# Kernel tuning notes

Measured on AMD Instinct MI355X. Metric: run time of the kernel, lower is better.

Reference implementation:

```python
import jax, jax.numpy as jnp
import numpy as np
from jax import lax

M, B, L, Q, S = 4, 64, 512, 512, 26  # models, batch, seq_len, hmm states, alphabet


def setup_inputs() -> dict:
    key = jax.random.key(0)
    k1, k2, k3, k4 = jax.random.split(key, 4)
    inputs = jax.random.uniform(k1, (M, B, L, S), dtype=jnp.float32)
    A_logits = jax.random.normal(k2, (M, Q, Q), dtype=jnp.float32)
    init_logits = jax.random.normal(k3, (M, Q), dtype=jnp.float32)
    em_logits = jax.random.normal(k4, (M, Q, S), dtype=jnp.float32)
    return {"inputs": inputs, "A_logits": A_logits,
            "init_logits": init_logits, "em_logits": em_logits}


def reference(inputs, A_logits, init_logits, em_logits):
    """Profile-HMM forward algorithm (scaled), as run by the MsaHmmCell RNN.

    inputs:      [M, B, L, S] observation probabilities (one-hot or soft)
    A_logits:    [M, Q, Q]    transition logits (row-softmax -> stochastic A)
    init_logits: [M, Q]       initial state distribution logits
    em_logits:   [M, Q, S]    emission logits (softmax over alphabet)
    returns loglik [M, B]  (the tensor the layer returns)
    """
    A = jax.nn.softmax(A_logits, axis=-1)        # [M, Q, Q]
    pi = jax.nn.softmax(init_logits, axis=-1)    # [M, Q]
    Bem = jax.nn.softmax(em_logits, axis=-1)     # [M, Q, S]

    # per-step emission likelihoods, time-major for scan: [L, M, B, Q]
    E = jnp.einsum('mbls,mqs->lmbq', inputs, Bem)

    # t = 0: alpha_0 = pi * e_0, scaled
    a0 = pi[:, None, :] * E[0]                   # [M, B, Q]
    s0 = jnp.sum(a0, axis=-1, keepdims=True)
    carry0 = (a0 / s0, jnp.log(s0[..., 0]))      # (alpha [M,B,Q], loglik [M,B])

    def step(carry, e_t):
        alpha, ll = carry
        r = jnp.einsum('mbq,mqp->mbp', alpha, A)  # transition
        a = r * e_t                               # emission
        s = jnp.sum(a, axis=-1, keepdims=True)    # scaling factor
        return (a / s, ll + jnp.log(s[..., 0])), None

    (alpha, loglik), _ = lax.scan(step, carry0, E[1:])
    return loglik  # [M, B] == reshape(loglik, (num_models, -1)) in the layer
```

## Files before the change

kernel.cpp:

```cpp
#include <hip/hip_runtime.h>
#include <hip/hip_bf16.h>
#include <math.h>


#define MM 4
#define BB 64
#define LL 512
#define QQ 512
#define SS 26
#define ASTR 528

typedef float f32x4 __attribute__((ext_vector_type(4)));
typedef int i32x4 __attribute__((ext_vector_type(4)));
typedef int i32x8 __attribute__((ext_vector_type(8)));

__device__ __forceinline__ float bf2f(unsigned short u) {
    return __uint_as_float(((unsigned)u) << 16);
}
__device__ __forceinline__ unsigned short f2bf(float f) {
    unsigned u = __float_as_uint(f);
    u = u + 0x7FFFu + ((u >> 16) & 1u);
    return (unsigned short)(u >> 16);
}
__device__ __forceinline__ unsigned char f2fp8(float x) {
    int r = __builtin_amdgcn_cvt_pk_fp8_f32(x, x, 0, false);
    return (unsigned char)(r & 0xFF);
}
__device__ __forceinline__ i32x8 ld32B(const unsigned char* p) {
    i32x4 lo = *(const i32x4*)p;
    i32x4 hi = *(const i32x4*)(p + 16);
    return __builtin_shufflevector(lo, hi, 0, 1, 2, 3, 4, 5, 6, 7);
}
__device__ __forceinline__ void barrier_lds() {
    __asm__ __volatile__("" ::: "memory");
    __builtin_amdgcn_s_waitcnt(0xC07F);
    __builtin_amdgcn_s_barrier();
    __asm__ __volatile__("" ::: "memory");
}


__global__ void prep_small(const float* __restrict__ il, const float* __restrict__ em,
                           float* __restrict__ pi, float* __restrict__ Bem) {
    int blk = blockIdx.x;
    int m = blk / (QQ + 1);
    int r = blk % (QQ + 1);
    int lane = threadIdx.x;
    if (r < QQ) {
        float x = (lane < SS) ? em[((size_t)m * QQ + r) * SS + lane] : -1e30f;
        float mx = x;
        #pragma unroll
        for (int o = 1; o < 64; o <<= 1) mx = fmaxf(mx, __shfl_xor(mx, o));
        float e = (lane < SS) ? __expf(x - mx) : 0.f;
        float s = e;
        #pragma unroll
        for (int o = 1; o < 64; o <<= 1) s += __shfl_xor(s, o);
        if (lane < SS) Bem[((size_t)m * QQ + r) * SS + lane] = e / s;
    } else {
        float v[8];
        float mx = -1e30f;
        #pragma unroll
        for (int k = 0; k < 8; ++k) { v[k] = il[m * QQ + k * 64 + lane]; mx = fmaxf(mx, v[k]); }
        #pragma unroll
        for (int o = 1; o < 64; o <<= 1) mx = fmaxf(mx, __shfl_xor(mx, o));
        float s = 0.f;
        #pragma unroll
        for (int k = 0; k < 8; ++k) { v[k] = __expf(v[k] - mx); s += v[k]; }
        #pragma unroll
        for (int o = 1; o < 64; o <<= 1) s += __shfl_xor(s, o);
        #pragma unroll
        for (int k = 0; k < 8; ++k) pi[m * QQ + k * 64 + lane] = v[k] / s;
    }
}

__global__ void prep_arow(const float* __restrict__ Al, float* __restrict__ Lrow) {
    int row = blockIdx.x;
    int lane = threadIdx.x;
    const float* p = Al + (size_t)row * QQ;
    float v[8];
    float mx = -1e30f;
    #pragma unroll
    for (int k = 0; k < 8; ++k) { v[k] = p[k * 64 + lane]; mx = fmaxf(mx, v[k]); }
    #pragma unroll
    for (int o = 1; o < 64; o <<= 1) mx = fmaxf(mx, __shfl_xor(mx, o));
    float s = 0.f;
    #pragma unroll
    for (int k = 0; k < 8; ++k) s += __expf(v[k] - mx);
    #pragma unroll
    for (int o = 1; o < 64; o <<= 1) s += __shfl_xor(s, o);
    if (lane == 0) Lrow[row] = mx + __logf(s);
}

__global__ void prep_atq(const float* __restrict__ Al, const float* __restrict__ Lrow,
                         unsigned char* __restrict__ Atq) {
    int bid = blockIdx.x;
    int m = bid >> 3, pb = bid & 7;
    __shared__ unsigned char tile[64][68];
    int l6 = threadIdx.x & 63, g = threadIdx.x >> 6;
    for (int c = 0; c < 8; ++c) {
        #pragma unroll
        for (int r = 0; r < 16; ++r) {
            int ql = g * 16 + r;
            int q = c * 64 + ql;
            float x = Al[((size_t)m * QQ + q) * QQ + pb * 64 + l6];
            tile[ql][l6] = f2fp8(__expf(x - Lrow[m * QQ + q]) * 256.f);
        }
        __syncthreads();
        #pragma unroll
        for (int r = 0; r < 16; ++r) {
            int pr = g * 16 + r;
            Atq[((size_t)m * QQ + pb * 64 + pr) * QQ + c * 64 + l6] = tile[l6][pr];
        }
        __syncthreads();
    }
}

__global__ void prep_e(const float* __restrict__ inp, const float* __restrict__ Bem,
                       unsigned short* __restrict__ E) {
    int bid = blockIdx.x;
    int tc = bid & 7;
    int b = (bid >> 3) & 63;
    int m = bid >> 9;
    int q0 = threadIdx.x;
    float bem0[SS], bem1[SS];
    const float* bp = Bem + (size_t)m * QQ * SS;
    #pragma unroll
    for (int j = 0; j < SS; ++j) bem0[j] = bp[(size_t)q0 * SS + j];
    #pragma unroll
    for (int j = 0; j < SS; ++j) bem1[j] = bp[(size_t)(q0 + 256) * SS + j];
    const float* ip = inp + (((size_t)(m * BB + b)) * LL + tc * 64) * SS;
    for (int lt = 0; lt < 64; ++lt) {
        int t = tc * 64 + lt;
        float a0 = 0.f, a1 = 0.f;
        #pragma unroll
        for (int j = 0; j < SS; ++j) {
            float x = ip[lt * SS + j];
            a0 += x * bem0[j];
            a1 += x * bem1[j];
        }
        size_t o = (((size_t)m * LL + t) * BB + b) * QQ + q0;
        E[o] = f2bf(a0);
        E[o + 256] = f2bf(a1);
    }
}


__launch_bounds__(1024, 4)
__global__ void hmm_scan(const unsigned short* __restrict__ E,
                         const unsigned char* __restrict__ Atq,
                         const float* __restrict__ pi,
                         float* __restrict__ out) {
    const int c = blockIdx.x;
    const int m = c >> 2, bg = c & 3;
    const int tid = threadIdx.x;
    const int lane = tid & 63;
    const int wv = tid >> 6;
    const int sl = lane & 15;
    const int quad = lane >> 4;
    const float LOG256 = 5.545177444479562f;

    __shared__ unsigned char albuf[2][16 * ASTR];
    __shared__ float psl[2][16][36];
    __shared__ float Sfin[2][16];

    i32x8 breg[2][4];
    {
        const unsigned char* Ab = Atq + (size_t)m * QQ * QQ;
        #pragma unroll
        for (int h = 0; h < 2; ++h) {
            int p = wv * 32 + h * 16 + sl;
            const unsigned char* rp = Ab + (size_t)p * QQ + quad * 32;
            #pragma unroll
            for (int kc = 0; kc < 4; ++kc)
                breg[h][kc] = ld32B(rp + kc * 128);
        }
    }

    int wq[2];
    #pragma unroll
    for (int h = 0; h < 2; ++h)
        wq[h] = sl * ASTR + wv * 32 + h * 16 + quad * 4;

    const int b = bg * 16 + sl;
    const size_t ebase = (size_t)m * LL * BB * QQ;
    const ushort4* __restrict__ E4 = (const ushort4*)(E + ebase);
    const unsigned ESTR4 = (BB * QQ) >> 2;
    const unsigned ebq = (unsigned)(b * QQ) >> 2;
    const unsigned eoffs0 = (unsigned)(wv * 8 + quad);
    const unsigned eoffs1 = eoffs0 + 4;

    float v[2][4];
    ushort4 ea[2], eb[2];

    {
        ea[0] = E4[ebq + ESTR4 + eoffs0];
        ea[1] = E4[ebq + ESTR4 + eoffs1];
        #pragma unroll
        for (int h = 0; h < 2; ++h) {
            int p0 = wv * 32 + h * 16 + quad * 4;
            f32x4 pv = *(const f32x4*)(pi + m * QQ + p0);
            ushort4 e0 = E4[ebq + (h ? eoffs1 : eoffs0)];
            v[h][0] = pv[0] * bf2f(e0.x);
            v[h][1] = pv[1] * bf2f(e0.y);
            v[h][2] = pv[2] * bf2f(e0.z);
            v[h][3] = pv[3] * bf2f(e0.w);
        }
    }

    float lam = 0.5f;
    float gprev = 1.0f;
    float ll = 0.0f;

    auto body = [&](int t, ushort4 (&ecur)[2], ushort4 (&enxt)[2], unsigned epre) {
        const int par = t & 1;
        enxt[0] = E4[epre + eoffs0];
        enxt[1] = E4[epre + eoffs1];

        float g = 128.0f * __builtin_amdgcn_rcpf(lam);
        unsigned char* ab = &albuf[par][0];
        #pragma unroll
        for (int h = 0; h < 2; ++h) {
            int d = __builtin_amdgcn_cvt_pk_fp8_f32(g * v[h][0], g * v[h][1], 0, false);
            d = __builtin_amdgcn_cvt_pk_fp8_f32(g * v[h][2], g * v[h][3], d, true);
            *(int*)(ab + wq[h]) = d;
        }
        float ps = (v[0][0] + v[0][1]) + (v[0][2] + v[0][3])
                 + (v[1][0] + v[1][1]) + (v[1][2] + v[1][3]);
        ps += __shfl_xor(ps, 16);
        if ((quad & 1) == 0) psl[par][sl][2 * wv + (quad >> 1)] = ps;

        ll -= __logf(g) + LOG256;

        barrier_lds();

        if (wv == 0 && lane < 32) {
            const f32x4* pr = (const f32x4*)&psl[par][sl][(lane >> 4) * 16];
            f32x4 s0 = pr[0], s1 = pr[1], s2 = pr[2], s3 = pr[3];
            f32x4 ss4 = (s0 + s1) + (s2 + s3);
            float ss = (ss4[0] + ss4[1]) + (ss4[2] + ss4[3]);
            ss += __shfl_xor(ss, 16);
            if (lane < 16) Sfin[par][sl] = ss;
        }
        if (t == 0) {
            lam = 16384.0f;
        } else {
            float Sp = Sfin[par ^ 1][sl];
            lam = 16384.0f * g * gprev * Sp;
        }
        gprev = g;

        f32x4 acc[2];
        acc[0] = (f32x4){0.f, 0.f, 0.f, 0.f};
        acc[1] = (f32x4){0.f, 0.f, 0.f, 0.f};
        const unsigned char* ar = &albuf[par][0] + sl * ASTR + quad * 32;
        #pragma unroll
        for (int kc = 0; kc < 4; ++kc) {
            i32x8 af = ld32B(ar + kc * 128);
            #pragma unroll
            for (int h = 0; h < 2; ++h)
                acc[h] = __builtin_amdgcn_mfma_scale_f32_16x16x128_f8f6f4(
                    breg[h][kc], af, acc[h], 0, 0,
                    0, 0x7F7F7F7F, 0, 0x7F7F7F7F);
        }
        #pragma unroll
        for (int h = 0; h < 2; ++h) {
            v[h][0] = acc[h][0] * bf2f(ecur[h].x);
            v[h][1] = acc[h][1] * bf2f(ecur[h].y);
            v[h][2] = acc[h][2] * bf2f(ecur[h].z);
            v[h][3] = acc[h][3] * bf2f(ecur[h].w);
        }
    };

    unsigned epre = ebq + 2 * ESTR4;
    for (int t = 0; t < LL - 2; t += 2) {
        body(t, ea, eb, epre); epre += ESTR4;
        body(t + 1, eb, ea, epre); epre += ESTR4;
    }
    body(LL - 2, ea, eb, ebq + (unsigned)(LL - 1) * ESTR4);

    {
        float ps = (v[0][0] + v[0][1]) + (v[0][2] + v[0][3])
                 + (v[1][0] + v[1][1]) + (v[1][2] + v[1][3]);
        ps += __shfl_xor(ps, 16);
        if ((quad & 1) == 0) psl[1][sl][2 * wv + (quad >> 1)] = ps;
        __syncthreads();
        if (wv == 0 && lane < 16) {
            const f32x4* pr = (const f32x4*)&psl[1][sl][0];
            f32x4 s0 = (pr[0] + pr[1]) + (pr[2] + pr[3]);
            f32x4 s1 = (pr[4] + pr[5]) + (pr[6] + pr[7]);
            f32x4 ss = s0 + s1;
            float S = (ss[0] + ss[1]) + (ss[2] + ss[3]);
            out[m * BB + bg * 16 + sl] = ll + __logf(S);
        }
    }
}


extern "C" void kernel_launch(void* const* d_in, const int* in_sizes, int n_in,
                              void* d_out, int out_size, void* d_ws, size_t ws_size,
                              hipStream_t stream) {
    const float* inputs = (const float*)d_in[0];
    const float* A_logits = (const float*)d_in[1];
    const float* init_logits = (const float*)d_in[2];
    const float* em_logits = (const float*)d_in[3];
    float* out = (float*)d_out;

    char* ws = (char*)d_ws;
    size_t off = 0;
    unsigned short* E = (unsigned short*)(ws + off);  off += (size_t)MM * LL * BB * QQ * 2;
    unsigned char* Atq = (unsigned char*)(ws + off);  off += (size_t)MM * QQ * QQ;
    float* Bem = (float*)(ws + off);                  off += (size_t)MM * QQ * SS * 4;
    float* pi = (float*)(ws + off);                   off += (size_t)MM * QQ * 4;
    float* Lrow = (float*)(ws + off);                 off += (size_t)MM * QQ * 4;

    if (ws_size < off) {
        (void)hipMemsetAsync(d_out, 0, (size_t)out_size * sizeof(float), stream);
        return;
    }

    prep_small<<<dim3(MM * (QQ + 1)), dim3(64), 0, stream>>>(init_logits, em_logits, pi, Bem);
    prep_arow<<<dim3(MM * QQ), dim3(64), 0, stream>>>(A_logits, Lrow);
    prep_atq<<<dim3(MM * 8), dim3(256), 0, stream>>>(A_logits, Lrow, Atq);
    prep_e<<<dim3(MM * BB * 8), dim3(256), 0, stream>>>(inputs, Bem, E);
    hmm_scan<<<dim3(16), dim3(1024), 0, stream>>>(E, Atq, pi, out);
}
```

Before: 608.8 us.

## Halve scan block to 8 waves, each computing 64 output states

The recurrent scan kernel now uses 512 threads (8 waves) per block instead of 1024. Each wave holds four 16-row slices of the fp8 transition matrix in registers and issues four MFMAs per k-chunk rather than two. The partial-sum reduction over waves shrinks from 32 to 16 entries per batch column, which simplifies the per-step reduction. The aim is cheaper per-step barriers and reductions plus more MFMA work per wave, at the cost of higher register pressure and half as many waves to hide latency.

```diff
diff --git a/kernel.cpp b/kernel.cpp
--- a/kernel.cpp
+++ b/kernel.cpp
@@ -144,7 +144,7 @@
 }
 
 
-__launch_bounds__(1024, 4)
+__launch_bounds__(512, 2)
 __global__ void hmm_scan(const unsigned short* __restrict__ E,
                          const unsigned char* __restrict__ Atq,
                          const float* __restrict__ pi,
@@ -159,15 +159,15 @@
     const float LOG256 = 5.545177444479562f;
 
     __shared__ unsigned char albuf[2][16 * ASTR];
-    __shared__ float psl[2][16][36];
+    __shared__ __align__(16) float psl[2][16][20];
     __shared__ float Sfin[2][16];
 
-    i32x8 breg[2][4];
+    i32x8 breg[4][4];
     {
         const unsigned char* Ab = Atq + (size_t)m * QQ * QQ;
         #pragma unroll
-        for (int h = 0; h < 2; ++h) {
-            int p = wv * 32 + h * 16 + sl;
+        for (int h = 0; h < 4; ++h) {
+            int p = wv * 64 + h * 16 + sl;
             const unsigned char* rp = Ab + (size_t)p * QQ + quad * 32;
             #pragma unroll
             for (int kc = 0; kc < 4; ++kc)
@@ -175,30 +175,31 @@
         }
     }
 
-    int wq[2];
-    #pragma unroll
-    for (int h = 0; h < 2; ++h)
-        wq[h] = sl * ASTR + wv * 32 + h * 16 + quad * 4;
+    int wq[4];
+    #pragma unroll
+    for (int h = 0; h < 4; ++h)
+        wq[h] = sl * ASTR + wv * 64 + h * 16 + quad * 4;
 
     const int b = bg * 16 + sl;
     const size_t ebase = (size_t)m * LL * BB * QQ;
     const ushort4* __restrict__ E4 = (const ushort4*)(E + ebase);
     const unsigned ESTR4 = (BB * QQ) >> 2;
     const unsigned ebq = (unsigned)(b * QQ) >> 2;
-    const unsigned eoffs0 = (unsigned)(wv * 8 + quad);
-    const unsigned eoffs1 = eoffs0 + 4;
-
-    float v[2][4];
-    ushort4 ea[2], eb[2];
+    unsigned eoffs[4];
+    #pragma unroll
+    for (int h = 0; h < 4; ++h) eoffs[h] = (unsigned)(wv * 16 + h * 4 + quad);
+
+    float v[4][4];
+    ushort4 ea[4], eb[4];
 
     {
-        ea[0] = E4[ebq + ESTR4 + eoffs0];
-        ea[1] = E4[ebq + ESTR4 + eoffs1];
-        #pragma unroll
-        for (int h = 0; h < 2; ++h) {
-            int p0 = wv * 32 + h * 16 + quad * 4;
+        #pragma unroll
+        for (int h = 0; h < 4; ++h) ea[h] = E4[ebq + ESTR4 + eoffs[h]];
+        #pragma unroll
+        for (int h = 0; h < 4; ++h) {
+            int p0 = wv * 64 + h * 16 + quad * 4;
             f32x4 pv = *(const f32x4*)(pi + m * QQ + p0);
-            ushort4 e0 = E4[ebq + (h ? eoffs1 : eoffs0)];
+            ushort4 e0 = E4[ebq + eoffs[h]];
             v[h][0] = pv[0] * bf2f(e0.x);
             v[h][1] = pv[1] * bf2f(e0.y);
             v[h][2] = pv[2] * bf2f(e0.z);
@@ -210,21 +211,23 @@
     float gprev = 1.0f;
     float ll = 0.0f;
 
-    auto body = [&](int t, ushort4 (&ecur)[2], ushort4 (&enxt)[2], unsigned epre) {
+    auto body = [&](int t, ushort4 (&ecur)[4], ushort4 (&enxt)[4], unsigned epre) {
         const int par = t & 1;
-        enxt[0] = E4[epre + eoffs0];
-        enxt[1] = E4[epre + eoffs1];
+        #pragma unroll
+        for (int h = 0; h < 4; ++h) enxt[h] = E4[epre + eoffs[h]];
 
         float g = 128.0f * __builtin_amdgcn_rcpf(lam);
         unsigned char* ab = &albuf[par][0];
         #pragma unroll
-        for (int h = 0; h < 2; ++h) {
+        for (int h = 0; h < 4; ++h) {
             int d = __builtin_amdgcn_cvt_pk_fp8_f32(g * v[h][0], g * v[h][1], 0, false);
             d = __builtin_amdgcn_cvt_pk_fp8_f32(g * v[h][2], g * v[h][3], d, true);
             *(int*)(ab + wq[h]) = d;
         }
-        float ps = (v[0][0] + v[0][1]) + (v[0][2] + v[0][3])
-                 + (v[1][0] + v[1][1]) + (v[1][2] + v[1][3]);
+        float ps = ((v[0][0] + v[0][1]) + (v[0][2] + v[0][3]))
+                 + ((v[1][0] + v[1][1]) + (v[1][2] + v[1][3]))
+                 + ((v[2][0] + v[2][1]) + (v[2][2] + v[2][3]))
+                 + ((v[3][0] + v[3][1]) + (v[3][2] + v[3][3]));
         ps += __shfl_xor(ps, 16);
         if ((quad & 1) == 0) psl[par][sl][2 * wv + (quad >> 1)] = ps;
 
@@ -232,13 +235,10 @@
 
         barrier_lds();
 
-        if (wv == 0 && lane < 32) {
-            const f32x4* pr = (const f32x4*)&psl[par][sl][(lane >> 4) * 16];
-            f32x4 s0 = pr[0], s1 = pr[1], s2 = pr[2], s3 = pr[3];
-            f32x4 ss4 = (s0 + s1) + (s2 + s3);
-            float ss = (ss4[0] + ss4[1]) + (ss4[2] + ss4[3]);
-            ss += __shfl_xor(ss, 16);
-            if (lane < 16) Sfin[par][sl] = ss;
+        if (wv == 0 && lane < 16) {
+            const f32x4* pr = (const f32x4*)&psl[par][lane][0];
+            f32x4 ss4 = (pr[0] + pr[1]) + (pr[2] + pr[3]);
+            Sfin[par][lane] = (ss4[0] + ss4[1]) + (ss4[2] + ss4[3]);
         }
         if (t == 0) {
             lam = 16384.0f;
@@ -248,21 +248,21 @@
         }
         gprev = g;
 
-        f32x4 acc[2];
-        acc[0] = (f32x4){0.f, 0.f, 0.f, 0.f};
-        acc[1] = (f32x4){0.f, 0.f, 0.f, 0.f};
+        f32x4 acc[4];
+        #pragma unroll
+        for (int h = 0; h < 4; ++h) acc[h] = (f32x4){0.f, 0.f, 0.f, 0.f};
         const unsigned char* ar = &albuf[par][0] + sl * ASTR + quad * 32;
         #pragma unroll
         for (int kc = 0; kc < 4; ++kc) {
             i32x8 af = ld32B(ar + kc * 128);
             #pragma unroll
-            for (int h = 0; h < 2; ++h)
+            for (int h = 0; h < 4; ++h)
                 acc[h] = __builtin_amdgcn_mfma_scale_f32_16x16x128_f8f6f4(
                     breg[h][kc], af, acc[h], 0, 0,
                     0, 0x7F7F7F7F, 0, 0x7F7F7F7F);
         }
         #pragma unroll
-        for (int h = 0; h < 2; ++h) {
+        for (int h = 0; h < 4; ++h) {
             v[h][0] = acc[h][0] * bf2f(ecur[h].x);
             v[h][1] = acc[h][1] * bf2f(ecur[h].y);
             v[h][2] = acc[h][2] * bf2f(ecur[h].z);
@@ -278,18 +278,18 @@
     body(LL - 2, ea, eb, ebq + (unsigned)(LL - 1) * ESTR4);
 
     {
-        float ps = (v[0][0] + v[0][1]) + (v[0][2] + v[0][3])
-                 + (v[1][0] + v[1][1]) + (v[1][2] + v[1][3]);
+        float ps = ((v[0][0] + v[0][1]) + (v[0][2] + v[0][3]))
+                 + ((v[1][0] + v[1][1]) + (v[1][2] + v[1][3]))
+                 + ((v[2][0] + v[2][1]) + (v[2][2] + v[2][3]))
+                 + ((v[3][0] + v[3][1]) + (v[3][2] + v[3][3]));
         ps += __shfl_xor(ps, 16);
         if ((quad & 1) == 0) psl[1][sl][2 * wv + (quad >> 1)] = ps;
         __syncthreads();
         if (wv == 0 && lane < 16) {
-            const f32x4* pr = (const f32x4*)&psl[1][sl][0];
-            f32x4 s0 = (pr[0] + pr[1]) + (pr[2] + pr[3]);
-            f32x4 s1 = (pr[4] + pr[5]) + (pr[6] + pr[7]);
-            f32x4 ss = s0 + s1;
-            float S = (ss[0] + ss[1]) + (ss[2] + ss[3]);
-            out[m * BB + bg * 16 + sl] = ll + __logf(S);
+            const f32x4* pr = (const f32x4*)&psl[1][lane][0];
+            f32x4 ss4 = (pr[0] + pr[1]) + (pr[2] + pr[3]);
+            float S = (ss4[0] + ss4[1]) + (ss4[2] + ss4[3]);
+            out[m * BB + bg * 16 + lane] = ll + __logf(S);
         }
     }
 }
@@ -321,5 +321,5 @@
     prep_arow<<<dim3(MM * QQ), dim3(64), 0, stream>>>(A_logits, Lrow);
     prep_atq<<<dim3(MM * 8), dim3(256), 0, stream>>>(A_logits, Lrow, Atq);
     prep_e<<<dim3(MM * BB * 8), dim3(256), 0, stream>>>(inputs, Bem, E);
-    hmm_scan<<<dim3(16), dim3(1024), 0, stream>>>(E, Atq, pi, out);
-}
+    hmm_scan<<<dim3(16), dim3(512), 0, stream>>>(E, Atq, pi, out);
+}
```

Result: faster. 591.1 us (-2.9%).
